# Optimization experiments

Hardware: AMD Instinct MI355X
Metric: run time of the kernel (lower is better)

## Reference

```python
import jax, jax.numpy as jnp
import numpy as np

B, N, TAPS, T = 64, 2000, 64, 2000


def setup_inputs() -> dict:
    key = jax.random.key(0)
    k1, k2 = jax.random.split(key)
    return {
        "x_seq": jax.random.normal(k1, (B, N, TAPS), dtype=jnp.float32),
        "d_seq": jax.random.normal(k2, (B, N), dtype=jnp.float32),
        # one learnable forgetting factor per unrolled RLS layer, init 0.99
        "lambdas": jnp.full((T,), 0.99, dtype=jnp.float32),
    }


def reference(x_seq, d_seq, lambdas):
    Bb, Nn, taps = x_seq.shape
    steps = min(lambdas.shape[0], Nn)
    w0 = jnp.zeros((Bb, taps), dtype=x_seq.dtype)
    P0 = jnp.broadcast_to(jnp.eye(taps, dtype=x_seq.dtype), (Bb, taps, taps))

    # time-major inputs for lax.scan
    xs = (jnp.swapaxes(x_seq[:, :steps, :], 0, 1),  # (steps, B, taps)
          jnp.swapaxes(d_seq[:, :steps], 0, 1),     # (steps, B)
          lambdas[:steps])                           # (steps,)

    def step(carry, inp):
        w, P = carry
        x, d, lam = inp
        lam = jnp.clip(lam, 1e-4, 0.9999)
        Px = jnp.einsum('bij,bj->bi', P, x)                 # (B, taps)
        denom = lam + jnp.einsum('bi,bi->b', x, Px)          # (B,)
        g = Px / denom[:, None]                              # gain (B, taps)
        y_hat = jnp.sum(w * x, axis=-1)                      # (B,)
        w_next = w + g * (d - y_hat)[:, None]
        xP = jnp.einsum('bj,bjk->bk', x, P)                  # x^T P, (B, taps)
        P_next = (P - g[:, :, None] * xP[:, None, :]) / lam  # rank-1 downdate
        return (w_next, P_next), y_hat

    (w_final, P_final), y_hats = jax.lax.scan(step, (w0, P0), xs)
    return jnp.swapaxes(y_hats, 0, 1), w_final  # (B, steps), (B, taps)
```

## Files before the change

### kernel.cpp

```cpp
#include <hip/hip_runtime.h>


#define B_ 64
#define N_ 2000
#define TAPS_ 64
#define STEPS_ 2000
#define VST_ 72

typedef float f2 __attribute__((ext_vector_type(2)));

__device__ __forceinline__ f2 pk2(float v) { f2 r; r.x = v; r.y = v; return r; }

__device__ __forceinline__ void lds_barrier() {
    asm volatile("s_waitcnt lgkmcnt(0)\n\ts_barrier" ::: "memory");
}

__device__ __forceinline__ float clipl(float v) {
    return fminf(fmaxf(v, 1e-4f), 0.9999f);
}

__device__ __forceinline__ float quad_reduce(float v) {
    int t1 = __builtin_amdgcn_update_dpp(__float_as_int(v), __float_as_int(v),
                                         0xB1, 0xF, 0xF, false);
    v += __int_as_float(t1);
    int t2 = __builtin_amdgcn_update_dpp(__float_as_int(v), __float_as_int(v),
                                         0x4E, 0xF, 0xF, false);
    v += __int_as_float(t2);
    return v;
}

__device__ __forceinline__ float rcp_nr(float v) {
    float r = __builtin_amdgcn_rcpf(v);
    float e = fmaf(-v, r, 1.0f);
    return fmaf(r, e, r);
}

__global__ __launch_bounds__(256, 1) void rls_kernel(
    const float* __restrict__ x_seq,
    const float* __restrict__ d_seq,
    const float* __restrict__ lambdas,
    float* __restrict__ y_out,
    float* __restrict__ w_out)
{
    const int b   = blockIdx.x;
    const int tid = threadIdx.x;
    const int r   = tid >> 2;
    const int q   = tid & 3;
    const int qb  = q << 4;

    __shared__ __align__(16) float  bufs[2][4][VST_];
    __shared__ __align__(16) float  d_lds[STEPS_];
    __shared__ __align__(16) float2 lam2[STEPS_];

    const float* xb = x_seq + (size_t)b * N_ * TAPS_;
    const float* db = d_seq + (size_t)b * N_;

    for (int idx = tid; idx < STEPS_; idx += 256) {
        d_lds[idx] = db[idx];
        const float lc = clipl(lambdas[idx]);
        lam2[idx] = make_float2(lc, rcp_nr(lc));
    }

    f2 Q[8], QT[8], w[8];
    #pragma unroll
    for (int j = 0; j < 8; ++j) {
        Q[j].x = (qb + 2*j     == r) ? 1.0f : 0.0f;
        Q[j].y = (qb + 2*j + 1 == r) ? 1.0f : 0.0f;
        QT[j] = Q[j];
        w[j]  = pk2(0.0f);
    }
    float sig = 1.0f;

    auto unpack4 = [](f2* dst, float4 v) {
        dst[0].x = v.x; dst[0].y = v.y; dst[1].x = v.z; dst[1].y = v.w;
    };

    auto loadpair = [&](f2 (&dA)[8], f2 (&dB)[8], int row) {
        const float4* v0 = (const float4*)(xb + (size_t)row * TAPS_ + qb);
        const float4* v1 = (const float4*)(xb + (size_t)(row + 1) * TAPS_ + qb);
        #pragma unroll
        for (int j4 = 0; j4 < 4; ++j4) {
            unpack4(&dA[2*j4], v0[j4]);
            unpack4(&dB[2*j4], v1[j4]);
        }
    };

    f2 P0a[8], P0b[8], P1a[8], P1b[8], P2a[8], P2b[8], P3a[8], P3b[8];
    loadpair(P0a, P0b, 0);
    loadpair(P1a, P1b, 2);
    loadpair(P2a, P2b, 4);

    float qxrS, xqrS, urS, vrS, wy0S, wy1S;

    {
        f2 qx2 = pk2(0.f), xq2 = pk2(0.f), u2 = pk2(0.f), v2 = pk2(0.f);
        #pragma unroll
        for (int j = 0; j < 8; ++j) {
            qx2 = __builtin_elementwise_fma(Q[j],  P0a[j], qx2);
            xq2 = __builtin_elementwise_fma(QT[j], P0a[j], xq2);
            u2  = __builtin_elementwise_fma(Q[j],  P0b[j], u2);
            v2  = __builtin_elementwise_fma(QT[j], P0b[j], v2);
        }
        qxrS = quad_reduce(qx2.x + qx2.y);
        xqrS = quad_reduce(xq2.x + xq2.y);
        urS  = quad_reduce(u2.x + u2.y);
        vrS  = quad_reduce(v2.x + v2.y);
        bufs[0][q][r] = (q == 0) ? qxrS : (q == 1) ? xqrS : (q == 2) ? urS : vrS;

        f2 wy02 = pk2(0.f), wy12 = pk2(0.f);
        #pragma unroll
        for (int j = 0; j < 8; ++j) {
            wy02 = __builtin_elementwise_fma(w[j], P0a[j], wy02);
            wy12 = __builtin_elementwise_fma(w[j], P0b[j], wy12);
        }
        wy0S = quad_reduce(wy02.x + wy02.y);
        wy1S = quad_reduce(wy12.x + wy12.y);
    }

    auto round = [&](int t, f2 (&x0)[8], f2 (&x1)[8],
                     f2 (&xn0)[8], f2 (&xn1)[8],
                     f2 (&xf0)[8], f2 (&xf1)[8],
                     int par, bool pf, bool fuse)
    {
        lds_barrier();

        const float2 l0 = lam2[t];
        const float2 l1 = lam2[t + 1];
        const float2 dd = *(const float2*)&d_lds[t];

        if (pf) loadpair(xf0, xf1, t + 6);

        f2 Qxq[8], xQq[8], uq[8], vq[8];
        {
            const float4* p0 = (const float4*)(&bufs[par][0][qb]);
            const float4* p1 = (const float4*)(&bufs[par][1][qb]);
            const float4* p2 = (const float4*)(&bufs[par][2][qb]);
            const float4* p3 = (const float4*)(&bufs[par][3][qb]);
            #pragma unroll
            for (int j4 = 0; j4 < 4; ++j4) {
                unpack4(&Qxq[2*j4], p0[j4]);
                unpack4(&xQq[2*j4], p1[j4]);
                unpack4(&uq [2*j4], p2[j4]);
                unpack4(&vq [2*j4], p3[j4]);
            }
        }

        f2 pd2 = pk2(0.f), a2 = pk2(0.f), bb2 = pk2(0.f), c22 = pk2(0.f);
        #pragma unroll
        for (int j = 0; j < 8; ++j) {
            pd2 = __builtin_elementwise_fma(x0[j], Qxq[j], pd2);
            a2  = __builtin_elementwise_fma(x1[j], xQq[j], a2);
            bb2 = __builtin_elementwise_fma(x1[j], Qxq[j], bb2);
            c22 = __builtin_elementwise_fma(x1[j], uq[j],  c22);
        }
        const float pd0 = quad_reduce(pd2.x + pd2.y);
        const float a   = quad_reduce(a2.x + a2.y);
        const float bb  = quad_reduce(bb2.x + bb2.y);
        const float c2  = quad_reduce(c22.x + c22.y);

        const float den0 = fmaf(sig, pd0, l0.x);
        const float s0   = sig * rcp_nr(den0);
        const float err0 = dd.x - wy0S;
        const float es0  = s0 * err0;
        const float sa   = s0 * a;
        const float sb   = s0 * bb;

        const float sig1 = sig * l0.y;
        const float pd1  = fmaf(-sa, bb, c2);
        const float den1 = fmaf(sig1, pd1, l1.x);
        const float s1   = sig1 * rcp_nr(den1);
        const float y1   = fmaf(es0, bb, wy1S);
        const float err1 = dd.y - y1;
        const float es1  = s1 * err1;
        sig = sig1 * l1.y;

        if (tid == 0)
            *(float2*)(y_out + (size_t)b * N_ + t) = make_float2(wy0S, y1);

        const float qx1r = fmaf(-sa, qxrS, urS);
        const float xq1r = fmaf(-sb, xqrS, vrS);
        const f2 nsa   = pk2(-sa);
        const f2 nsb   = pk2(-sb);
        const f2 s0v   = pk2(s0);
        const f2 s1v   = pk2(s1);
        const f2 es0v  = pk2(es0);
        const f2 es1v  = pk2(es1);
        const f2 ntr0  = pk2(-(s0 * qxrS));
        const f2 ntr1  = pk2(-(s1 * qx1r));
        const f2 nxqr  = pk2(-xqrS);
        const f2 nxq1r = pk2(-xq1r);

        f2 nqx = pk2(0.f), nxq = pk2(0.f), nu = pk2(0.f), nv = pk2(0.f);
        f2 nw0 = pk2(0.f), nw1 = pk2(0.f);

        #pragma unroll
        for (int j = 0; j < 8; ++j) {
            const f2 Qx1 = __builtin_elementwise_fma(nsa, Qxq[j], uq[j]);
            const f2 xQ1 = __builtin_elementwise_fma(nsb, xQq[j], vq[j]);
            const f2 tq0 = s0v * Qxq[j];
            const f2 tq1 = s1v * Qx1;
            w[j] = __builtin_elementwise_fma(Qxq[j], es0v, w[j]);
            w[j] = __builtin_elementwise_fma(Qx1,    es1v, w[j]);
            Q[j] = __builtin_elementwise_fma(ntr0, xQq[j], Q[j]);
            Q[j] = __builtin_elementwise_fma(ntr1, xQ1,    Q[j]);
            QT[j] = __builtin_elementwise_fma(tq0, nxqr,  QT[j]);
            QT[j] = __builtin_elementwise_fma(tq1, nxq1r, QT[j]);
            if (fuse) {
                nqx = __builtin_elementwise_fma(Q[j],  xn0[j], nqx);
                nxq = __builtin_elementwise_fma(QT[j], xn0[j], nxq);
                nu  = __builtin_elementwise_fma(Q[j],  xn1[j], nu);
                nv  = __builtin_elementwise_fma(QT[j], xn1[j], nv);
                nw0 = __builtin_elementwise_fma(w[j],  xn0[j], nw0);
                nw1 = __builtin_elementwise_fma(w[j],  xn1[j], nw1);
            }
        }

        if (fuse) {
            qxrS = quad_reduce(nqx.x + nqx.y);
            xqrS = quad_reduce(nxq.x + nxq.y);
            urS  = quad_reduce(nu.x + nu.y);
            vrS  = quad_reduce(nv.x + nv.y);
            bufs[par ^ 1][q][r] =
                (q == 0) ? qxrS : (q == 1) ? xqrS : (q == 2) ? urS : vrS;
            wy0S = quad_reduce(nw0.x + nw0.y);
            wy1S = quad_reduce(nw1.x + nw1.y);
        }
    };

    for (int t = 0; t < 1992; t += 8) {
        round(t + 0, P0a, P0b, P1a, P1b, P3a, P3b, 0, true, true);
        round(t + 2, P1a, P1b, P2a, P2b, P0a, P0b, 1, true, true);
        round(t + 4, P2a, P2b, P3a, P3b, P1a, P1b, 0, true, true);
        round(t + 6, P3a, P3b, P0a, P0b, P2a, P2b, 1, true, true);
    }
    round(1992, P0a, P0b, P1a, P1b, P3a, P3b, 0, true,  true);
    round(1994, P1a, P1b, P2a, P2b, P0a, P0b, 1, false, true);
    round(1996, P2a, P2b, P3a, P3b, P1a, P1b, 0, false, true);
    round(1998, P3a, P3b, P0a, P0b, P2a, P2b, 1, false, false);

    if (r == 0) {
        float4* wo = (float4*)(w_out + (size_t)b * TAPS_ + qb);
        #pragma unroll
        for (int j4 = 0; j4 < 4; ++j4)
            wo[j4] = make_float4(w[2*j4].x, w[2*j4].y, w[2*j4+1].x, w[2*j4+1].y);
    }
}

extern "C" void kernel_launch(void* const* d_in, const int* in_sizes, int n_in,
                              void* d_out, int out_size, void* d_ws, size_t ws_size,
                              hipStream_t stream) {
    const float* x_seq   = (const float*)d_in[0];
    const float* d_seq   = (const float*)d_in[1];
    const float* lambdas = (const float*)d_in[2];

    float* y_out = (float*)d_out;
    float* w_out = (float*)d_out + (size_t)B_ * N_;

    rls_kernel<<<B_, 256, 0, stream>>>(x_seq, d_seq, lambdas, y_out, w_out);
}
```

Measured before the change: 941.6 us.

## Defer weight update to next round and reorder dot products off critical path

The weight update and the w·x prediction dot products move out of the end of each round into the start of the next round. Previous gain vectors and error scalars are kept in registers to do this. The pd0 reduction and reciprocal are split out first so the denominator computation can start earlier, and the global prefetch of future x rows is moved after the scalar chain. The aim is to shorten the serial dependency chain between barriers and overlap memory loads with compute, at the cost of more live registers (16 extra f2 values), which risks register pressure or spills.

```diff
diff --git a/kernel.cpp b/kernel.cpp
--- a/kernel.cpp
+++ b/kernel.cpp
@@ -90,7 +90,13 @@
     loadpair(P1a, P1b, 2);
     loadpair(P2a, P2b, 4);
 
-    float qxrS, xqrS, urS, vrS, wy0S, wy1S;
+    float qxrS, xqrS, urS, vrS;
+    float wy0S, wy1S;
+
+    f2 Qxq_p[8], Qx1_p[8];
+    f2 es0v_p = pk2(0.0f), es1v_p = pk2(0.0f);
+    #pragma unroll
+    for (int j = 0; j < 8; ++j) { Qxq_p[j] = pk2(0.0f); Qx1_p[j] = pk2(0.0f); }
 
     {
         f2 qx2 = pk2(0.f), xq2 = pk2(0.f), u2 = pk2(0.f), v2 = pk2(0.f);
@@ -106,15 +112,6 @@
         urS  = quad_reduce(u2.x + u2.y);
         vrS  = quad_reduce(v2.x + v2.y);
         bufs[0][q][r] = (q == 0) ? qxrS : (q == 1) ? xqrS : (q == 2) ? urS : vrS;
-
-        f2 wy02 = pk2(0.f), wy12 = pk2(0.f);
-        #pragma unroll
-        for (int j = 0; j < 8; ++j) {
-            wy02 = __builtin_elementwise_fma(w[j], P0a[j], wy02);
-            wy12 = __builtin_elementwise_fma(w[j], P0b[j], wy12);
-        }
-        wy0S = quad_reduce(wy02.x + wy02.y);
-        wy1S = quad_reduce(wy12.x + wy12.y);
     }
 
     auto round = [&](int t, f2 (&x0)[8], f2 (&x1)[8],
@@ -123,12 +120,6 @@
                      int par, bool pf, bool fuse)
     {
         lds_barrier();
-
-        const float2 l0 = lam2[t];
-        const float2 l1 = lam2[t + 1];
-        const float2 dd = *(const float2*)&d_lds[t];
-
-        if (pf) loadpair(xf0, xf1, t + 6);
 
         f2 Qxq[8], xQq[8], uq[8], vq[8];
         {
@@ -144,22 +135,40 @@
                 unpack4(&vq [2*j4], p3[j4]);
             }
         }
-
-        f2 pd2 = pk2(0.f), a2 = pk2(0.f), bb2 = pk2(0.f), c22 = pk2(0.f);
-        #pragma unroll
-        for (int j = 0; j < 8; ++j) {
+        const float2 l0 = lam2[t];
+        const float2 l1 = lam2[t + 1];
+        const float2 dd = *(const float2*)&d_lds[t];
+
+        f2 nw0 = pk2(0.f), nw1 = pk2(0.f);
+        #pragma unroll
+        for (int j = 0; j < 8; ++j) {
+            w[j] = __builtin_elementwise_fma(Qxq_p[j], es0v_p, w[j]);
+            w[j] = __builtin_elementwise_fma(Qx1_p[j], es1v_p, w[j]);
+            nw0  = __builtin_elementwise_fma(w[j], x0[j], nw0);
+            nw1  = __builtin_elementwise_fma(w[j], x1[j], nw1);
+        }
+        wy0S = quad_reduce(nw0.x + nw0.y);
+        wy1S = quad_reduce(nw1.x + nw1.y);
+
+        f2 pd2 = pk2(0.f);
+        #pragma unroll
+        for (int j = 0; j < 8; ++j)
             pd2 = __builtin_elementwise_fma(x0[j], Qxq[j], pd2);
+        const float pd0  = quad_reduce(pd2.x + pd2.y);
+        const float den0 = fmaf(sig, pd0, l0.x);
+        const float s0   = sig * rcp_nr(den0);
+
+        f2 a2 = pk2(0.f), bb2 = pk2(0.f), c22 = pk2(0.f);
+        #pragma unroll
+        for (int j = 0; j < 8; ++j) {
             a2  = __builtin_elementwise_fma(x1[j], xQq[j], a2);
             bb2 = __builtin_elementwise_fma(x1[j], Qxq[j], bb2);
             c22 = __builtin_elementwise_fma(x1[j], uq[j],  c22);
         }
-        const float pd0 = quad_reduce(pd2.x + pd2.y);
         const float a   = quad_reduce(a2.x + a2.y);
         const float bb  = quad_reduce(bb2.x + bb2.y);
         const float c2  = quad_reduce(c22.x + c22.y);
 
-        const float den0 = fmaf(sig, pd0, l0.x);
-        const float s0   = sig * rcp_nr(den0);
         const float err0 = dd.x - wy0S;
         const float es0  = s0 * err0;
         const float sa   = s0 * a;
@@ -177,21 +186,20 @@
         if (tid == 0)
             *(float2*)(y_out + (size_t)b * N_ + t) = make_float2(wy0S, y1);
 
+        if (pf) loadpair(xf0, xf1, t + 6);
+
         const float qx1r = fmaf(-sa, qxrS, urS);
         const float xq1r = fmaf(-sb, xqrS, vrS);
         const f2 nsa   = pk2(-sa);
         const f2 nsb   = pk2(-sb);
         const f2 s0v   = pk2(s0);
         const f2 s1v   = pk2(s1);
-        const f2 es0v  = pk2(es0);
-        const f2 es1v  = pk2(es1);
         const f2 ntr0  = pk2(-(s0 * qxrS));
         const f2 ntr1  = pk2(-(s1 * qx1r));
         const f2 nxqr  = pk2(-xqrS);
         const f2 nxq1r = pk2(-xq1r);
 
         f2 nqx = pk2(0.f), nxq = pk2(0.f), nu = pk2(0.f), nv = pk2(0.f);
-        f2 nw0 = pk2(0.f), nw1 = pk2(0.f);
 
         #pragma unroll
         for (int j = 0; j < 8; ++j) {
@@ -199,8 +207,6 @@
             const f2 xQ1 = __builtin_elementwise_fma(nsb, xQq[j], vq[j]);
             const f2 tq0 = s0v * Qxq[j];
             const f2 tq1 = s1v * Qx1;
-            w[j] = __builtin_elementwise_fma(Qxq[j], es0v, w[j]);
-            w[j] = __builtin_elementwise_fma(Qx1,    es1v, w[j]);
             Q[j] = __builtin_elementwise_fma(ntr0, xQq[j], Q[j]);
             Q[j] = __builtin_elementwise_fma(ntr1, xQ1,    Q[j]);
             QT[j] = __builtin_elementwise_fma(tq0, nxqr,  QT[j]);
@@ -210,10 +216,12 @@
                 nxq = __builtin_elementwise_fma(QT[j], xn0[j], nxq);
                 nu  = __builtin_elementwise_fma(Q[j],  xn1[j], nu);
                 nv  = __builtin_elementwise_fma(QT[j], xn1[j], nv);
-                nw0 = __builtin_elementwise_fma(w[j],  xn0[j], nw0);
-                nw1 = __builtin_elementwise_fma(w[j],  xn1[j], nw1);
             }
-        }
+            Qxq_p[j] = Qxq[j];
+            Qx1_p[j] = Qx1;
+        }
+        es0v_p = pk2(es0);
+        es1v_p = pk2(es1);
 
         if (fuse) {
             qxrS = quad_reduce(nqx.x + nqx.y);
@@ -222,8 +230,6 @@
             vrS  = quad_reduce(nv.x + nv.y);
             bufs[par ^ 1][q][r] =
                 (q == 0) ? qxrS : (q == 1) ? xqrS : (q == 2) ? urS : vrS;
-            wy0S = quad_reduce(nw0.x + nw0.y);
-            wy1S = quad_reduce(nw1.x + nw1.y);
         }
     };
 
@@ -237,6 +243,12 @@
     round(1994, P1a, P1b, P2a, P2b, P0a, P0b, 1, false, true);
     round(1996, P2a, P2b, P3a, P3b, P1a, P1b, 0, false, true);
     round(1998, P3a, P3b, P0a, P0b, P2a, P2b, 1, false, false);
+
+    #pragma unroll
+    for (int j = 0; j < 8; ++j) {
+        w[j] = __builtin_elementwise_fma(Qxq_p[j], es0v_p, w[j]);
+        w[j] = __builtin_elementwise_fma(Qx1_p[j], es1v_p, w[j]);
+    }
 
     if (r == 0) {
         float4* wo = (float4*)(w_out + (size_t)b * TAPS_ + qb);
```

Result: slower. 1.006 ms (+6.8%).
